# Optimization experiments

Measured on AMD Instinct MI355X. Metric: run time of the kernel, lower is better.

The kernel has to match this reference:

```python
import jax, jax.numpy as jnp
import numpy as np


def setup_inputs() -> dict:
    key = jax.random.key(0)
    ks = jax.random.split(key, 8)
    B, L, F, H, A = 128, 196, 2048, 512, 512
    features = jax.random.normal(ks[0], (B, L, F), dtype=jnp.float32)
    hidden_state = jax.random.normal(ks[1], (B, H), dtype=jnp.float32)
    # Linear params (PyTorch layout: weight [out, in], bias [out]); scaled like kaiming-uniform
    W_enc = jax.random.normal(ks[2], (A, F), dtype=jnp.float32) / np.sqrt(F)
    b_enc = jnp.zeros((A,), dtype=jnp.float32)
    W_dec = jax.random.normal(ks[3], (A, H), dtype=jnp.float32) / np.sqrt(H)
    b_dec = jnp.zeros((A,), dtype=jnp.float32)
    W_com = jax.random.normal(ks[4], (1, A), dtype=jnp.float32) / np.sqrt(A)
    b_com = jnp.zeros((1,), dtype=jnp.float32)
    return {
        "features": features, "hidden_state": hidden_state,
        "W_enc": W_enc, "b_enc": b_enc,
        "W_dec": W_dec, "b_dec": b_dec,
        "W_com": W_com, "b_com": b_com,
    }


def reference(features, hidden_state, W_enc, b_enc, W_dec, b_dec, W_com, b_com):
    # encoder_context: [B, L, A]
    enc = jnp.einsum('blf,af->bla', features, W_enc) + b_enc
    # decoder_context: [B, 1, A]
    dec = (hidden_state @ W_dec.T + b_dec)[:, None, :]
    # relu + linear to scalar score (dropout in eval mode = identity): [B, L]
    scores = jnp.einsum('bla,a->bl', jax.nn.relu(enc + dec), W_com[0]) + b_com[0]
    alpha = jax.nn.softmax(scores, axis=1)  # [B, L]
    weighted_features = jnp.einsum('blf,bl->bf', features, alpha)  # [B, F]
    return weighted_features, alpha
```

## Files before the change

### kernel.cpp

```cpp
#include <hip/hip_runtime.h>
#include <hip/hip_bf16.h>
#include <math.h>

#define B_  128
#define L_  196
#define F_  2048
#define H_  512
#define A_  512
#define ML_ (B_*L_)

typedef _Float16 half8 __attribute__((ext_vector_type(8)));
typedef _Float16 half4v __attribute__((ext_vector_type(4)));
typedef _Float16 half2v __attribute__((ext_vector_type(2)));
typedef float f32x4 __attribute__((ext_vector_type(4)));

__device__ __forceinline__ void gld_lds16(const void* g, void* l) {
  __builtin_amdgcn_global_load_lds((const __attribute__((address_space(1))) void*)g,
                                   (__attribute__((address_space(3))) void*)l, 16, 0, 0);
}

__global__ __launch_bounds__(256) void k_prep(const float4* __restrict__ Wenc4,
                                              half4v* __restrict__ wH,
                                              const float* __restrict__ hs,
                                              const float* __restrict__ Wdec,
                                              const float* __restrict__ bdec,
                                              const float* __restrict__ benc,
                                              float* __restrict__ dec,
                                              float* __restrict__ scores) {
  const int b = blockIdx.x, t = threadIdx.x;

  {
    const int base = b * 2048 + t;
    float4 v[8];
#pragma unroll
    for (int j = 0; j < 8; j++) v[j] = Wenc4[base + j * 256];
#pragma unroll
    for (int j = 0; j < 8; j++) {
      half4v o = { (_Float16)v[j].x, (_Float16)v[j].y, (_Float16)v[j].z, (_Float16)v[j].w };
      wH[base + j * 256] = o;
    }
  }

  const int g = b * 256 + t;
  if (g < ML_) scores[g] = 0.f;

  __shared__ float h[H_];
  h[t]       = hs[b * H_ + t];
  h[t + 256] = hs[b * H_ + t + 256];
  __syncthreads();

#pragma unroll
  for (int r = 0; r < 2; r++) {
    const int a = t + r * 256;
    float acc = bdec[a] + benc[a];
    const float4* wr = (const float4*)(Wdec + (size_t)a * H_);
#pragma unroll 4
    for (int k4 = 0; k4 < H_ / 4; k4++) {
      const float4 w = wr[k4];
      acc += w.x * h[4*k4] + w.y * h[4*k4+1] + w.z * h[4*k4+2] + w.w * h[4*k4+3];
    }
    dec[b * A_ + a] = acc;
  }
}

__global__ __launch_bounds__(256) void k_scores_mfma(const float* __restrict__ fA,
                                                     const _Float16* __restrict__ fB,
                                                     const float* __restrict__ dec,
                                                     const float* __restrict__ wcom,
                                                     float* __restrict__ scores) {
  __shared__ _Float16  As[128 * 64];
  __shared__ _Float16  Bs[2][128 * 64];
  __shared__ float decS[2][128];

  const int tid  = threadIdx.x;
  const int lane = tid & 63;
  const int w    = tid >> 6;

  const int l = blockIdx.x;
  int at_, mt;
  if (l < 768) { at_ = (l >> 3) & 3; mt = (l >> 5) * 8 + (l & 7); }
  else { const int idx = l - 768; at_ = idx >> 2; mt = 192 + (idx & 3); }
  const int a0 = at_ * 128;
  const int m0 = mt * 128;

  const int wm   = w & 1;
  const int wn   = w >> 1;
  const int quad = lane >> 4;
  const int l16  = lane & 15;

  f32x4 acc[4][4];
#pragma unroll
  for (int i = 0; i < 4; i++)
#pragma unroll
    for (int j = 0; j < 4; j++)
#pragma unroll
      for (int k = 0; k < 4; k++) acc[i][j][k] = 0.f;

  const int b0 = m0 / L_;
  {
    const int i = tid >> 7;
    const int j = tid & 127;
    int bb = b0 + i; if (bb > B_ - 1) bb = B_ - 1;
    decS[i][j] = dec[bb * A_ + a0 + j];
  }

  const int arow4 = lane >> 4;
  const int acol  = (lane & 15) * 4;
  const float* pA = fA + (size_t)(m0 + w * 32 + arow4) * F_ + acol;
  const int g8    = lane & 15;

  const int srowB = lane >> 3;
  const _Float16* pB = fB + (size_t)(a0 + w * 32 + srowB) * F_
                          + (size_t)(((lane & 7) ^ srowB) * 8);

  float4 fr[8];
#pragma unroll
  for (int i = 0; i < 8; i++)
    fr[i] = *(const float4*)(pA + (size_t)(i * 4) * F_);
#pragma unroll
  for (int i = 0; i < 4; i++)
    gld_lds16(pB + (size_t)(i * 8) * F_, &Bs[0][(w * 32 + i * 8) * 64]);

  auto kstep = [&](int kt, int buf, bool last) {
#pragma unroll
    for (int i = 0; i < 8; i++) {
      const int r = w * 32 + i * 4 + arow4;
      half4v h;
      half2v h0 = (half2v)__builtin_amdgcn_cvt_pkrtz(fr[i].x, fr[i].y);
      half2v h1 = (half2v)__builtin_amdgcn_cvt_pkrtz(fr[i].z, fr[i].w);
      h[0] = h0[0]; h[1] = h0[1]; h[2] = h1[0]; h[3] = h1[1];
      *(half4v*)&As[r * 64 + (g8 ^ ((r & 7) << 1)) * 4] = h;
    }
    if (!last) {
#pragma unroll
      for (int i = 0; i < 8; i++)
        fr[i] = *(const float4*)(pA + (size_t)(i * 4) * F_ + kt + 64);
#pragma unroll
      for (int i = 0; i < 4; i++)
        gld_lds16(pB + (size_t)(i * 8) * F_ + kt + 64,
                  &Bs[buf ^ 1][(w * 32 + i * 8) * 64]);
      asm volatile("s_waitcnt vmcnt(12) lgkmcnt(0)" ::: "memory");
    } else {
      asm volatile("s_waitcnt vmcnt(0) lgkmcnt(0)" ::: "memory");
    }
    __builtin_amdgcn_s_barrier();
    __builtin_amdgcn_sched_barrier(0);

#pragma unroll
    for (int kk = 0; kk < 2; kk++) {
      half8 af[4], bf[4];
#pragma unroll
      for (int mf = 0; mf < 4; mf++) {
        const int row = wm * 64 + mf * 16 + l16;
        af[mf] = *(const half8*)&As[row * 64 + (((kk * 4 + quad)) ^ (row & 7)) * 8];
      }
#pragma unroll
      for (int at = 0; at < 4; at++) {
        const int row = wn * 64 + at * 16 + l16;
        bf[at] = *(const half8*)&Bs[buf][row * 64 + (((kk * 4 + quad)) ^ (row & 7)) * 8];
      }
#pragma unroll
      for (int mf = 0; mf < 4; mf++)
#pragma unroll
        for (int at = 0; at < 4; at++)
          acc[mf][at] = __builtin_amdgcn_mfma_f32_16x16x32_f16(af[mf], bf[at], acc[mf][at], 0, 0, 0);
    }

    __builtin_amdgcn_sched_barrier(0);
    __builtin_amdgcn_s_barrier();
    __builtin_amdgcn_sched_barrier(0);
  };

  int kt = 0;
  for (int s = 0; s < 31; ++s, kt += 64) kstep(kt, s & 1, false);
  kstep(kt, 31 & 1, true);

  float w4[4];
#pragma unroll
  for (int at = 0; at < 4; at++) w4[at] = wcom[a0 + wn * 64 + at * 16 + l16];

#pragma unroll
  for (int mf = 0; mf < 4; mf++) {
#pragma unroll
    for (int r = 0; r < 4; r++) {
      const int m  = m0 + wm * 64 + mf * 16 + quad * 4 + r;
      const int db = m / L_ - b0;
      float p = 0.f;
#pragma unroll
      for (int at = 0; at < 4; at++) {
        const float e = acc[mf][at][r] + decS[db][wn * 64 + at * 16 + l16];
        p = fmaf(fmaxf(e, 0.f), w4[at], p);
      }
      p += __shfl_xor(p, 1);
      p += __shfl_xor(p, 2);
      p += __shfl_xor(p, 4);
      p += __shfl_xor(p, 8);
      if (l16 == 0) atomicAdd(&scores[m], p);
    }
  }
}

__global__ __launch_bounds__(256) void k_softmax(const float* __restrict__ scores,
                                                 float* __restrict__ alpha) {
  const int b = blockIdx.x, t = threadIdx.x;
  __shared__ float redm[4];
  __shared__ float reds[4];

  float s = (t < L_) ? scores[b * L_ + t] : -INFINITY;
  float m = s;
#pragma unroll
  for (int o = 32; o >= 1; o >>= 1) m = fmaxf(m, __shfl_xor(m, o));
  if ((t & 63) == 0) redm[t >> 6] = m;
  __syncthreads();
  m = fmaxf(fmaxf(redm[0], redm[1]), fmaxf(redm[2], redm[3]));
  float e = (t < L_) ? expf(s - m) : 0.f;
  float sum = e;
#pragma unroll
  for (int o = 32; o >= 1; o >>= 1) sum += __shfl_xor(sum, o);
  if ((t & 63) == 0) reds[t >> 6] = sum;
  __syncthreads();
  sum = reds[0] + reds[1] + reds[2] + reds[3];
  if (t < L_) alpha[b * L_ + t] = e / sum;
}

__global__ __launch_bounds__(128) void k_attn_f32(const float* __restrict__ feat,
                                                  const float* __restrict__ alpha,
                                                  float* __restrict__ out) {
  const int fc = blockIdx.x, b = blockIdx.y, t = threadIdx.x;
  __shared__ float al[L_];

  al[t] = alpha[b * L_ + t];
  if (t < L_ - 128) al[t + 128] = alpha[b * L_ + t + 128];
  __syncthreads();

  const int f0 = fc * 256 + t * 2;
  const float2* fp = (const float2*)(feat + (size_t)b * L_ * F_ + f0);
  float a0x = 0.f, a0y = 0.f, a1x = 0.f, a1y = 0.f;
#pragma unroll 7
  for (int ll = 0; ll < 98; ll++) {
    const float2 v0 = fp[(size_t)ll * (F_ / 2)];
    const float2 v1 = fp[(size_t)(ll + 98) * (F_ / 2)];
    const float w0 = al[ll];
    const float w1 = al[ll + 98];
    a0x = fmaf(v0.x, w0, a0x);
    a0y = fmaf(v0.y, w0, a0y);
    a1x = fmaf(v1.x, w1, a1x);
    a1y = fmaf(v1.y, w1, a1y);
  }
  float2 o = { a0x + a1x, a0y + a1y };
  *(float2*)(out + (size_t)b * F_ + f0) = o;
}

__global__ __launch_bounds__(256) void k_scores_f32(const float* __restrict__ feat,
                                                    const float* __restrict__ Wenc,
                                                    const float* __restrict__ dec,
                                                    const float* __restrict__ wcom,
                                                    float* __restrict__ scores) {
  __shared__ float As[16][128];
  __shared__ float Bs[16][128];
  const int tid = threadIdx.x;
  const int m0 = blockIdx.x * 128;
  const int a0 = blockIdx.y * 128;
  const int tx = tid & 15;
  const int ty = tid >> 4;
  float acc[8][8];
#pragma unroll
  for (int i = 0; i < 8; i++)
#pragma unroll
    for (int j = 0; j < 8; j++) acc[i][j] = 0.f;
  for (int kt = 0; kt < F_; kt += 16) {
#pragma unroll
    for (int rep = 0; rep < 2; rep++) {
      const int idx = rep * 256 + tid;
      const int row = idx >> 2;
      const int kp  = (idx & 3) << 2;
      const float4 v = *(const float4*)(feat + (size_t)(m0 + row) * F_ + kt + kp);
      As[kp+0][row] = v.x; As[kp+1][row] = v.y; As[kp+2][row] = v.z; As[kp+3][row] = v.w;
      const float4 w = *(const float4*)(Wenc + (size_t)(a0 + row) * F_ + kt + kp);
      Bs[kp+0][row] = w.x; Bs[kp+1][row] = w.y; Bs[kp+2][row] = w.z; Bs[kp+3][row] = w.w;
    }
    __syncthreads();
#pragma unroll
    for (int k = 0; k < 16; k++) {
      float ar[8], br[8];
      *(float4*)&ar[0] = *(const float4*)&As[k][ty * 8];
      *(float4*)&ar[4] = *(const float4*)&As[k][ty * 8 + 4];
      *(float4*)&br[0] = *(const float4*)&Bs[k][tx * 8];
      *(float4*)&br[4] = *(const float4*)&Bs[k][tx * 8 + 4];
#pragma unroll
      for (int i = 0; i < 8; i++)
#pragma unroll
        for (int j = 0; j < 8; j++) acc[i][j] = fmaf(ar[i], br[j], acc[i][j]);
    }
    __syncthreads();
  }
  float w8[8];
  *(float4*)&w8[0] = *(const float4*)(wcom + a0 + tx * 8);
  *(float4*)&w8[4] = *(const float4*)(wcom + a0 + tx * 8 + 4);
#pragma unroll
  for (int i = 0; i < 8; i++) {
    const int m = m0 + ty * 8 + i;
    const int b = m / L_;
    const float* dp = dec + b * A_ + a0 + tx * 8;
    float p = 0.f;
#pragma unroll
    for (int j = 0; j < 8; j++) {
      const float e = acc[i][j] + dp[j];
      p = fmaf(fmaxf(e, 0.f), w8[j], p);
    }
    p += __shfl_xor(p, 1);
    p += __shfl_xor(p, 2);
    p += __shfl_xor(p, 4);
    p += __shfl_xor(p, 8);
    if (tx == 0) atomicAdd(&scores[m], p);
  }
}

__global__ __launch_bounds__(256) void k_dec_only(const float* __restrict__ hs,
                                                  const float* __restrict__ Wdec,
                                                  const float* __restrict__ bdec,
                                                  const float* __restrict__ benc,
                                                  float* __restrict__ dec,
                                                  float* __restrict__ scores) {
  const int b = blockIdx.x, t = threadIdx.x;
  const int g = b * 256 + t;
  if (g < ML_) scores[g] = 0.f;
  __shared__ float h[H_];
  h[t]       = hs[b * H_ + t];
  h[t + 256] = hs[b * H_ + t + 256];
  __syncthreads();
#pragma unroll
  for (int r = 0; r < 2; r++) {
    const int a = t + r * 256;
    float acc = bdec[a] + benc[a];
    const float4* wr = (const float4*)(Wdec + (size_t)a * H_);
#pragma unroll 4
    for (int k4 = 0; k4 < H_ / 4; k4++) {
      const float4 w = wr[k4];
      acc += w.x * h[4*k4] + w.y * h[4*k4+1] + w.z * h[4*k4+2] + w.w * h[4*k4+3];
    }
    dec[b * A_ + a] = acc;
  }
}

extern "C" void kernel_launch(void* const* d_in, const int* in_sizes, int n_in,
                              void* d_out, int out_size, void* d_ws, size_t ws_size,
                              hipStream_t stream) {
  const float* feat = (const float*)d_in[0];
  const float* hs   = (const float*)d_in[1];
  const float* Wenc = (const float*)d_in[2];
  const float* benc = (const float*)d_in[3];
  const float* Wdec = (const float*)d_in[4];
  const float* bdec = (const float*)d_in[5];
  const float* wcom = (const float*)d_in[6];

  float* out   = (float*)d_out;
  float* alpha = out + B_ * F_;
  float* dec    = (float*)d_ws;
  float* scores = dec + B_ * A_;

  const size_t need = (size_t)(B_ * A_ + ML_) * 4 + (size_t)A_ * F_ * 2;

  if (ws_size >= need) {
    _Float16* wH = (_Float16*)(scores + ML_);
    k_prep<<<dim3(128), dim3(256), 0, stream>>>(
        (const float4*)Wenc, (half4v*)wH, hs, Wdec, bdec, benc, dec, scores);
    k_scores_mfma<<<dim3(784), dim3(256), 0, stream>>>(feat, wH, dec, wcom, scores);
  } else {
    k_dec_only<<<dim3(B_), dim3(256), 0, stream>>>(hs, Wdec, bdec, benc, dec, scores);
    k_scores_f32<<<dim3(ML_ / 128, A_ / 128), dim3(256), 0, stream>>>(feat, Wenc, dec, wcom, scores);
  }
  k_softmax<<<dim3(B_), dim3(256), 0, stream>>>(scores, alpha);
  k_attn_f32<<<dim3(8, B_), dim3(128), 0, stream>>>(feat, alpha, out);
}
```

Before: 428.1 us.

## Halve scores GEMM A-tile to 64 columns and raise occupancy

The MFMA score kernel now processes 64 attention columns per block instead of 128, doubling the grid and halving accumulators and B-tile LDS, with launch bounds requesting higher occupancy. The decoder context is read directly from global memory in the epilogue instead of staged in LDS, and the explicit vmcnt wait is removed. The prep kernel is split across twice as many blocks. This trades more redundant reads of the fp32 feature tiles for more concurrent waves to hide latency.

```diff
diff --git a/kernel.cpp b/kernel.cpp
--- a/kernel.cpp
+++ b/kernel.cpp
@@ -27,21 +27,22 @@
                                               const float* __restrict__ benc,
                                               float* __restrict__ dec,
                                               float* __restrict__ scores) {
-  const int b = blockIdx.x, t = threadIdx.x;
+  const int bid = blockIdx.x, t = threadIdx.x;
+  const int b = bid >> 1, half = bid & 1;
 
   {
-    const int base = b * 2048 + t;
-    float4 v[8];
-#pragma unroll
-    for (int j = 0; j < 8; j++) v[j] = Wenc4[base + j * 256];
-#pragma unroll
-    for (int j = 0; j < 8; j++) {
+    const int base = bid * 1024 + t;
+    float4 v[4];
+#pragma unroll
+    for (int j = 0; j < 4; j++) v[j] = Wenc4[base + j * 256];
+#pragma unroll
+    for (int j = 0; j < 4; j++) {
       half4v o = { (_Float16)v[j].x, (_Float16)v[j].y, (_Float16)v[j].z, (_Float16)v[j].w };
       wH[base + j * 256] = o;
     }
   }
 
-  const int g = b * 256 + t;
+  const int g = bid * 256 + t;
   if (g < ML_) scores[g] = 0.f;
 
   __shared__ float h[H_];
@@ -49,9 +50,8 @@
   h[t + 256] = hs[b * H_ + t + 256];
   __syncthreads();
 
-#pragma unroll
-  for (int r = 0; r < 2; r++) {
-    const int a = t + r * 256;
+  {
+    const int a = half * 256 + t;
     float acc = bdec[a] + benc[a];
     const float4* wr = (const float4*)(Wdec + (size_t)a * H_);
 #pragma unroll 4
@@ -63,24 +63,23 @@
   }
 }
 
-__global__ __launch_bounds__(256) void k_scores_mfma(const float* __restrict__ fA,
-                                                     const _Float16* __restrict__ fB,
-                                                     const float* __restrict__ dec,
-                                                     const float* __restrict__ wcom,
-                                                     float* __restrict__ scores) {
+__global__ __launch_bounds__(256, 4) void k_scores_mfma(const float* __restrict__ fA,
+                                                        const _Float16* __restrict__ fB,
+                                                        const float* __restrict__ dec,
+                                                        const float* __restrict__ wcom,
+                                                        float* __restrict__ scores) {
   __shared__ _Float16  As[128 * 64];
-  __shared__ _Float16  Bs[2][128 * 64];
-  __shared__ float decS[2][128];
+  __shared__ _Float16  Bs[2][64 * 64];
 
   const int tid  = threadIdx.x;
   const int lane = tid & 63;
   const int w    = tid >> 6;
 
   const int l = blockIdx.x;
-  int at_, mt;
-  if (l < 768) { at_ = (l >> 3) & 3; mt = (l >> 5) * 8 + (l & 7); }
-  else { const int idx = l - 768; at_ = idx >> 2; mt = 192 + (idx & 3); }
-  const int a0 = at_ * 128;
+  int mt, c;
+  if (l < 1536) { mt = (l >> 6) * 8 + (l & 7); c = (l >> 3) & 7; }
+  else { const int idx = l - 1536; mt = 192 + (idx & 3); c = idx >> 2; }
+  const int a0 = c * 64;
   const int m0 = mt * 128;
 
   const int wm   = w & 1;
@@ -88,21 +87,13 @@
   const int quad = lane >> 4;
   const int l16  = lane & 15;
 
-  f32x4 acc[4][4];
+  f32x4 acc[4][2];
 #pragma unroll
   for (int i = 0; i < 4; i++)
 #pragma unroll
-    for (int j = 0; j < 4; j++)
+    for (int j = 0; j < 2; j++)
 #pragma unroll
       for (int k = 0; k < 4; k++) acc[i][j][k] = 0.f;
-
-  const int b0 = m0 / L_;
-  {
-    const int i = tid >> 7;
-    const int j = tid & 127;
-    int bb = b0 + i; if (bb > B_ - 1) bb = B_ - 1;
-    decS[i][j] = dec[bb * A_ + a0 + j];
-  }
 
   const int arow4 = lane >> 4;
   const int acol  = (lane & 15) * 4;
@@ -110,18 +101,26 @@
   const int g8    = lane & 15;
 
   const int srowB = lane >> 3;
-  const _Float16* pB = fB + (size_t)(a0 + w * 32 + srowB) * F_
+  const _Float16* pB = fB + (size_t)(a0 + w * 16 + srowB) * F_
                           + (size_t)(((lane & 7) ^ srowB) * 8);
 
+#pragma unroll
+  for (int i = 0; i < 2; i++)
+    gld_lds16(pB + (size_t)(i * 8) * F_, &Bs[0][(w * 16 + i * 8) * 64]);
   float4 fr[8];
 #pragma unroll
   for (int i = 0; i < 8; i++)
     fr[i] = *(const float4*)(pA + (size_t)(i * 4) * F_);
-#pragma unroll
-  for (int i = 0; i < 4; i++)
-    gld_lds16(pB + (size_t)(i * 8) * F_, &Bs[0][(w * 32 + i * 8) * 64]);
-
-  auto kstep = [&](int kt, int buf, bool last) {
+
+  for (int s = 0; s < 32; ++s) {
+    const int kt  = s * 64;
+    const int buf = s & 1;
+    if (s < 31) {
+#pragma unroll
+      for (int i = 0; i < 2; i++)
+        gld_lds16(pB + (size_t)(i * 8) * F_ + kt + 64,
+                  &Bs[buf ^ 1][(w * 16 + i * 8) * 64]);
+    }
 #pragma unroll
     for (int i = 0; i < 8; i++) {
       const int r = w * 32 + i * 4 + arow4;
@@ -131,65 +130,55 @@
       h[0] = h0[0]; h[1] = h0[1]; h[2] = h1[0]; h[3] = h1[1];
       *(half4v*)&As[r * 64 + (g8 ^ ((r & 7) << 1)) * 4] = h;
     }
-    if (!last) {
+    if (s < 31) {
 #pragma unroll
       for (int i = 0; i < 8; i++)
         fr[i] = *(const float4*)(pA + (size_t)(i * 4) * F_ + kt + 64);
-#pragma unroll
-      for (int i = 0; i < 4; i++)
-        gld_lds16(pB + (size_t)(i * 8) * F_ + kt + 64,
-                  &Bs[buf ^ 1][(w * 32 + i * 8) * 64]);
-      asm volatile("s_waitcnt vmcnt(12) lgkmcnt(0)" ::: "memory");
-    } else {
-      asm volatile("s_waitcnt vmcnt(0) lgkmcnt(0)" ::: "memory");
-    }
+    }
+    asm volatile("s_waitcnt lgkmcnt(0)" ::: "memory");
     __builtin_amdgcn_s_barrier();
     __builtin_amdgcn_sched_barrier(0);
 
 #pragma unroll
     for (int kk = 0; kk < 2; kk++) {
-      half8 af[4], bf[4];
+      half8 af[4], bf[2];
 #pragma unroll
       for (int mf = 0; mf < 4; mf++) {
         const int row = wm * 64 + mf * 16 + l16;
         af[mf] = *(const half8*)&As[row * 64 + (((kk * 4 + quad)) ^ (row & 7)) * 8];
       }
 #pragma unroll
-      for (int at = 0; at < 4; at++) {
-        const int row = wn * 64 + at * 16 + l16;
+      for (int at = 0; at < 2; at++) {
+        const int row = wn * 32 + at * 16 + l16;
         bf[at] = *(const half8*)&Bs[buf][row * 64 + (((kk * 4 + quad)) ^ (row & 7)) * 8];
       }
 #pragma unroll
       for (int mf = 0; mf < 4; mf++)
 #pragma unroll
-        for (int at = 0; at < 4; at++)
+        for (int at = 0; at < 2; at++)
           acc[mf][at] = __builtin_amdgcn_mfma_f32_16x16x32_f16(af[mf], bf[at], acc[mf][at], 0, 0, 0);
     }
 
     __builtin_amdgcn_sched_barrier(0);
     __builtin_amdgcn_s_barrier();
     __builtin_amdgcn_sched_barrier(0);
-  };
-
-  int kt = 0;
-  for (int s = 0; s < 31; ++s, kt += 64) kstep(kt, s & 1, false);
-  kstep(kt, 31 & 1, true);
-
-  float w4[4];
-#pragma unroll
-  for (int at = 0; at < 4; at++) w4[at] = wcom[a0 + wn * 64 + at * 16 + l16];
+  }
+
+  float w2[2];
+#pragma unroll
+  for (int at = 0; at < 2; at++) w2[at] = wcom[a0 + wn * 32 + at * 16 + l16];
 
 #pragma unroll
   for (int mf = 0; mf < 4; mf++) {
 #pragma unroll
     for (int r = 0; r < 4; r++) {
       const int m  = m0 + wm * 64 + mf * 16 + quad * 4 + r;
-      const int db = m / L_ - b0;
+      const int bb = m / L_;
       float p = 0.f;
 #pragma unroll
-      for (int at = 0; at < 4; at++) {
-        const float e = acc[mf][at][r] + decS[db][wn * 64 + at * 16 + l16];
-        p = fmaf(fmaxf(e, 0.f), w4[at], p);
+      for (int at = 0; at < 2; at++) {
+        const float e = acc[mf][at][r] + dec[bb * A_ + a0 + wn * 32 + at * 16 + l16];
+        p = fmaf(fmaxf(e, 0.f), w2[at], p);
       }
       p += __shfl_xor(p, 1);
       p += __shfl_xor(p, 2);
@@ -363,9 +352,9 @@
 
   if (ws_size >= need) {
     _Float16* wH = (_Float16*)(scores + ML_);
-    k_prep<<<dim3(128), dim3(256), 0, stream>>>(
+    k_prep<<<dim3(256), dim3(256), 0, stream>>>(
         (const float4*)Wenc, (half4v*)wH, hs, Wdec, bdec, benc, dec, scores);
-    k_scores_mfma<<<dim3(784), dim3(256), 0, stream>>>(feat, wH, dec, wcom, scores);
+    k_scores_mfma<<<dim3(1568), dim3(256), 0, stream>>>(feat, wH, dec, wcom, scores);
   } else {
     k_dec_only<<<dim3(B_), dim3(256), 0, stream>>>(hs, Wdec, bdec, benc, dec, scores);
     k_scores_f32<<<dim3(ML_ / 128, A_ / 128), dim3(256), 0, stream>>>(feat, Wenc, dec, wcom, scores);
```

Result: no change. 429.2 us (+0.3%).
